# Kernel tuning notes

Measured on AMD Instinct MI355X. Metric: run time of the kernel, lower is better.

Reference implementation:

```python
import jax, jax.numpy as jnp
from jax import lax
import numpy as np

H = 200           # mpnn_hidden_size
DEPTH = 3         # mpnn_depth
ATOM_FDIM = 39
BOND_FDIM = 11
B, NA, NB = 128, 48, 96   # molecules, atoms/mol, bonds/mol (padded fixed size)
L, VOCAB = 1000, 26       # protein length, amino-acid vocab
KERNALS = [3, 5, 7]
PROT_FILTERS = [50, 96, 128, 200]
FC_DIMS = [400, 200, 100, 1]


def setup_inputs() -> dict:
    key = jax.random.key(0)
    ks = jax.random.split(key, 32)
    s = 0.05
    inp = {}
    inp["fatoms"] = jax.random.normal(ks[0], (B, NA, ATOM_FDIM), jnp.float32)
    inp["fbonds"] = jax.random.normal(ks[1], (B, NB, ATOM_FDIM + BOND_FDIM), jnp.float32)
    inp["agraph"] = jax.random.randint(ks[2], (B, NA, 6), 0, NB)
    inp["bgraph"] = jax.random.randint(ks[3], (B, NB, 6), 0, NB)
    inp["protein_seq"] = jax.random.randint(ks[4], (B, L), 0, VOCAB)
    # MPNN weights (stored as (in, out) matrices; W_i and W_h have no bias)
    inp["W_i"] = jax.random.normal(ks[5], (ATOM_FDIM + BOND_FDIM, H), jnp.float32) * s
    inp["W_h"] = jax.random.normal(ks[6], (H, H), jnp.float32) * s
    inp["W_o_w"] = jax.random.normal(ks[7], (ATOM_FDIM + H, H), jnp.float32) * s
    inp["W_o_b"] = jax.random.normal(ks[8], (H,), jnp.float32) * s
    # protein embedding + CNN
    inp["embed_protein"] = jax.random.normal(ks[9], (VOCAB, PROT_FILTERS[0]), jnp.float32) * s
    for i, k in enumerate(KERNALS):
        inp[f"conv{i}_w"] = jax.random.normal(ks[10 + 2 * i], (PROT_FILTERS[i + 1], PROT_FILTERS[i], k), jnp.float32) * s
        inp[f"conv{i}_b"] = jax.random.normal(ks[11 + 2 * i], (PROT_FILTERS[i + 1],), jnp.float32) * s
    # CPI fc head 400 -> 200 -> 100 -> 1
    for i in range(3):
        inp[f"fc{i}_w"] = jax.random.normal(ks[16 + 2 * i], (FC_DIMS[i], FC_DIMS[i + 1]), jnp.float32) * s
        inp[f"fc{i}_b"] = jax.random.normal(ks[17 + 2 * i], (FC_DIMS[i + 1],), jnp.float32) * s
    return inp


def reference(fatoms, fbonds, agraph, bgraph, protein_seq,
              W_i, W_h, W_o_w, W_o_b, embed_protein,
              conv0_w, conv0_b, conv1_w, conv1_b, conv2_w, conv2_b,
              fc0_w, fc0_b, fc1_w, fc1_b, fc2_w, fc2_b):
    # ---- MPNN over all molecules (vmapped single_molecule_forward) ----
    def mol(fa, fb, ag, bg):
        binput = fb @ W_i                      # (NB, H)
        message = jax.nn.relu(binput)
        for _ in range(DEPTH - 1):
            nei = message[bg].sum(axis=1)      # gather (NB,6,H) -> sum -> (NB,H)
            message = jax.nn.relu(binput + nei @ W_h)
        nei = message[ag].sum(axis=1)          # (NA, H)
        atom_h = jax.nn.relu(jnp.concatenate([fa, nei], axis=1) @ W_o_w + W_o_b)
        return atom_h.mean(axis=0)             # (H,)

    embeddings = jax.vmap(mol)(fatoms, fbonds, agraph, bgraph)  # (B, H)

    # ---- protein CNN tower ----
    pv = embed_protein[protein_seq]            # (B, L, 50)
    pv = pv.transpose(0, 2, 1)                 # (B, 50, L)
    for w, b, k in ((conv0_w, conv0_b, KERNALS[0]),
                    (conv1_w, conv1_b, KERNALS[1]),
                    (conv2_w, conv2_b, KERNALS[2])):
        pv = lax.conv_general_dilated(pv, w, window_strides=(1,),
                                      padding=[(k // 2, k // 2)],
                                      dimension_numbers=("NCH", "OIH", "NCH"))
        pv = jax.nn.relu(pv + b[None, :, None])
    protein_vector = pv.max(axis=2)            # adaptive_max_pool1d(out=1) -> (B, 200)

    # ---- CPI fc head ----
    x = jnp.concatenate([embeddings, protein_vector], axis=1)  # (B, 400)
    x = jax.nn.relu(x @ fc0_w + fc0_b)
    x = jax.nn.relu(x @ fc1_w + fc1_b)
    x = x @ fc2_w + fc2_b
    return x                                   # (B, 1)
```

## Files before the change

kernel.cpp:

```cpp
#include <hip/hip_runtime.h>
#include <hip/hip_bf16.h>
#include <cstddef>

#define H 200
#define NA 48
#define NBB 96
#define BATCH 128
#define AFD 39
#define BFD 50
#define LP 1000
#define CATD (AFD + H)
#define APB 8
#define BIPB 16

typedef unsigned short ushort_t;
typedef __bf16 bf16x8 __attribute__((ext_vector_type(8)));
typedef float f32x16 __attribute__((ext_vector_type(16)));
typedef unsigned uint32x4 __attribute__((ext_vector_type(4)));

union U16B { uint4 u; bf16x8 b; };
static __device__ __forceinline__ bf16x8 as_bf16x8(uint4 u) { U16B x; x.u = u; return x.b; }
union U16B2 { uint32x4 u; bf16x8 b; };
static __device__ __forceinline__ bf16x8 as_bf16x8v(uint32x4 u) { U16B2 x; x.u = u; return x.b; }

static __device__ __forceinline__ ushort_t f2bf(float f) {
    union { float f; unsigned u; } a; a.f = f;
    unsigned r = (a.u + 0x7FFFu + ((a.u >> 16) & 1u)) >> 16;
    return (ushort_t)r;
}

static __device__ __forceinline__ uint32x4 gload16(const ushort_t* base, unsigned voff) {
    uint32x4 r;
    asm volatile("global_load_dwordx4 %0, %1, %2"
                 : "=&v"(r) : "v"(voff), "s"(base));
    return r;
}

template <int COUT, int CIN, int CP, int K>
static __device__ __forceinline__ void prep_one(int t, const float* __restrict__ w,
                                                ushort_t* __restrict__ Wb) {
    constexpr int NC = CP / 16;
    constexpr int NS = K * NC;
    int j = t & 7;
    int lane = (t >> 3) & 63;
    int s = (t >> 9) % NS;
    int ct = (t >> 9) / NS;
    int co = ct * 32 + (lane & 31);
    int tt = s / NC, cc = s % NC;
    int ci = cc * 16 + ((lane >> 5) & 1) * 8 + j;
    float v = 0.f;
    if (co < COUT && ci < CIN) v = w[((size_t)co * CIN + ci) * K + tt];
    Wb[t] = f2bf(v);
}

#define MNS 13
#define PREP_T0 (4 * 12 * 512)
#define PREP_T1 (PREP_T0 + 4 * 30 * 512)
#define PREP_T2 (PREP_T1 + 8 * 56 * 512)
#define PREP_T3 (PREP_T2 + 51200)
#define PREP_T4 (PREP_T3 + 8 * MNS * 512)
#define PREP_BLKS (PREP_T4 / 256)

static __device__ __forceinline__ void prep_body(
        int tid, const float* __restrict__ c0w, const float* __restrict__ c1w,
        const float* __restrict__ c2w, const float* __restrict__ Wh,
        float* __restrict__ x, ushort_t* __restrict__ Wb0,
        ushort_t* __restrict__ Wb1, ushort_t* __restrict__ Wb2,
        ushort_t* __restrict__ Wbh) {
    if (tid < PREP_T0) prep_one<96, 50, 64, 3>(tid, c0w, Wb0);
    else if (tid < PREP_T1) prep_one<128, 96, 96, 5>(tid - PREP_T0, c1w, Wb1);
    else if (tid < PREP_T2) prep_one<200, 128, 128, 7>(tid - PREP_T1, c2w, Wb2);
    else if (tid < PREP_T3) x[tid - PREP_T2] = 0.f;
    else if (tid < PREP_T4) {
        int t = tid - PREP_T3;
        int j = t & 7;
        int lane = (t >> 3) & 63;
        int s = (t >> 9) % MNS;
        int tile = (t >> 9) / MNS;
        int co = tile * 32 + (lane & 31);
        int ci = s * 16 + ((lane >> 5) & 1) * 8 + j;
        float v = 0.f;
        if (co < H && ci < H) v = Wh[ci * H + co];
        Wbh[t] = f2bf(v);
    }
}

template <int CP, int K, int COUT, int CO_WAVES, int L_WAVES, bool FMAX, bool EMB>
static __device__ __forceinline__ void conv_body(
        const ushort_t* __restrict__ act, const int* __restrict__ seq,
        const float* __restrict__ emb, const ushort_t* __restrict__ Wb,
        const float* __restrict__ bias, void* __restrict__ outv,
        ushort_t* __restrict__ Xs) {
    constexpr int NC = CP / 16;
    constexpr int NS = K * NC;
    constexpr int P = K / 2;
    constexpr int PITCH = CP + 8;
    constexpr int LTILE = 64 * L_WAVES;
    constexpr int ROWS = LTILE + K - 1;
    constexpr int CPR = CP / 8;
    constexpr int D = 4;

    int b = blockIdx.z, lb = blockIdx.x;
    int l0 = lb * LTILE;
    int tid = threadIdx.x;

    if (EMB) {
        const int* seqb = seq + (size_t)b * LP;
        for (int idx = tid; idx < ROWS * CPR; idx += 256) {
            int r = idx / CPR, c = idx % CPR;
            int l = l0 - P + r;
            uint4 v = {0u, 0u, 0u, 0u};
            if ((unsigned)l < (unsigned)LP) {
                int s = seqb[l];
                const float* e = emb + (size_t)s * 50;
                ushort_t h[8];
#pragma unroll
                for (int j = 0; j < 8; ++j) {
                    int cc = c * 8 + j;
                    h[j] = (cc < 50) ? f2bf(e[cc]) : (ushort_t)0;
                }
                v.x = (unsigned)h[0] | ((unsigned)h[1] << 16);
                v.y = (unsigned)h[2] | ((unsigned)h[3] << 16);
                v.z = (unsigned)h[4] | ((unsigned)h[5] << 16);
                v.w = (unsigned)h[6] | ((unsigned)h[7] << 16);
            }
            *(uint4*)(Xs + r * PITCH + c * 8) = v;
        }
    } else {
        const ushort_t* actb = act + (size_t)b * LP * CP;
        for (int idx = tid; idx < ROWS * CPR; idx += 256) {
            int r = idx / CPR, c = idx % CPR;
            int l = l0 - P + r;
            uint4 v = {0u, 0u, 0u, 0u};
            if ((unsigned)l < (unsigned)LP) v = *(const uint4*)(actb + (size_t)l * CP + c * 8);
            *(uint4*)(Xs + r * PITCH + c * 8) = v;
        }
    }

    int lane = tid & 63, wv = tid >> 6;
    int cw = wv % CO_WAVES, lw = wv / CO_WAVES;
    int ln31 = lane & 31, half = lane >> 5;

    unsigned abase0 = (unsigned)(cw * 2) * (unsigned)NS * 1024u + (unsigned)lane * 16u;
    unsigned abase1 = abase0 + (unsigned)NS * 1024u;
    int bbase = (lw * 64 + ln31) * PITCH + half * 8;

    f32x16 acc[2][2];
#pragma unroll
    for (int ct = 0; ct < 2; ++ct)
#pragma unroll
        for (int lt = 0; lt < 2; ++lt)
#pragma unroll
            for (int r = 0; r < 16; ++r) acc[ct][lt][r] = 0.f;

    __syncthreads();

    uint32x4 ra0[D], ra1[D];
#pragma unroll
    for (int d = 0; d < D; ++d) {
        ra0[d] = gload16(Wb, abase0 + (unsigned)(d * 1024));
        ra1[d] = gload16(Wb, abase1 + (unsigned)(d * 1024));
    }

    uint4 bC0 = *(const uint4*)(Xs + bbase);
    uint4 bC1 = *(const uint4*)(Xs + bbase + 32 * PITCH);

#pragma unroll
    for (int s = 0; s < NS; ++s) {
        int sn = (s + 1 < NS) ? s + 1 : NS - 1;
        int tn = sn / NC, ccn = sn % NC;
        int off = bbase + tn * PITCH + ccn * 16;
        uint4 bN0 = *(const uint4*)(Xs + off);
        uint4 bN1 = *(const uint4*)(Xs + off + 32 * PITCH);

        {
            const int rem = NS - 1 - s;
            const int allow = 2 * ((D - 1) < rem ? (D - 1) : rem);
            asm volatile("s_waitcnt vmcnt(%0)" :: "i"(allow) : "memory");
            __builtin_amdgcn_sched_barrier(0);
        }

        uint32x4 a0 = ra0[s % D];
        uint32x4 a1 = ra1[s % D];

        acc[0][0] = __builtin_amdgcn_mfma_f32_32x32x16_bf16(
            as_bf16x8v(a0), as_bf16x8(bC0), acc[0][0], 0, 0, 0);
        acc[1][0] = __builtin_amdgcn_mfma_f32_32x32x16_bf16(
            as_bf16x8v(a1), as_bf16x8(bC0), acc[1][0], 0, 0, 0);
        acc[0][1] = __builtin_amdgcn_mfma_f32_32x32x16_bf16(
            as_bf16x8v(a0), as_bf16x8(bC1), acc[0][1], 0, 0, 0);
        acc[1][1] = __builtin_amdgcn_mfma_f32_32x32x16_bf16(
            as_bf16x8v(a1), as_bf16x8(bC1), acc[1][1], 0, 0, 0);

        if (s + D < NS) {
            ra0[s % D] = gload16(Wb, abase0 + (unsigned)((s + D) * 1024));
            ra1[s % D] = gload16(Wb, abase1 + (unsigned)((s + D) * 1024));
        }

        bC0 = bN0; bC1 = bN1;
    }

    if (!FMAX) {
        ushort_t* out = (ushort_t*)outv + (size_t)b * LP * COUT;
#pragma unroll
        for (int ct = 0; ct < 2; ++ct) {
            int cbase = (cw * 2 + ct) * 32 + 4 * half;
#pragma unroll
            for (int g = 0; g < 4; ++g) {
                int co = cbase + 8 * g;
                if (co >= COUT) continue;
                float4 bv = *(const float4*)(bias + co);
#pragma unroll
                for (int lt = 0; lt < 2; ++lt) {
                    int l = l0 + lw * 64 + lt * 32 + ln31;
                    if (l < LP) {
                        ushort_t h0 = f2bf(fmaxf(acc[ct][lt][4 * g + 0] + bv.x, 0.f));
                        ushort_t h1 = f2bf(fmaxf(acc[ct][lt][4 * g + 1] + bv.y, 0.f));
                        ushort_t h2 = f2bf(fmaxf(acc[ct][lt][4 * g + 2] + bv.z, 0.f));
                        ushort_t h3 = f2bf(fmaxf(acc[ct][lt][4 * g + 3] + bv.w, 0.f));
                        uint2 o;
                        o.x = (unsigned)h0 | ((unsigned)h1 << 16);
                        o.y = (unsigned)h2 | ((unsigned)h3 << 16);
                        *(uint2*)(out + (size_t)l * COUT + co) = o;
                    }
                }
            }
        }
    } else {
        float* xout = (float*)outv;
#pragma unroll
        for (int ct = 0; ct < 2; ++ct) {
            float mx[16];
#pragma unroll
            for (int r = 0; r < 16; ++r) mx[r] = -3.0e38f;
#pragma unroll
            for (int lt = 0; lt < 2; ++lt) {
                int l = l0 + lw * 64 + lt * 32 + ln31;
                if (l < LP) {
#pragma unroll
                    for (int r = 0; r < 16; ++r) mx[r] = fmaxf(mx[r], acc[ct][lt][r]);
                }
            }
#pragma unroll
            for (int r = 0; r < 16; ++r) {
#pragma unroll
                for (int off = 1; off < 32; off <<= 1)
                    mx[r] = fmaxf(mx[r], __shfl_xor(mx[r], off, 64));
            }
            if (ln31 == 0) {
                int cbase = (cw * 2 + ct) * 32 + 4 * half;
#pragma unroll
                for (int r = 0; r < 16; ++r) {
                    int co = cbase + (r & 3) + 8 * (r >> 2);
                    if (co < COUT) {
                        float v = fmaxf(mx[r] + bias[co], 0.f);
                        atomicMax((int*)&xout[(size_t)b * 400 + 200 + co], __float_as_int(v));
                    }
                }
            }
        }
    }
}

#define MPITCH 216
static __device__ __forceinline__ void msg_body(
        int blk, const float* __restrict__ msgIn, const float* __restrict__ binput,
        const int* __restrict__ bgraph, const ushort_t* __restrict__ Wbh,
        float* __restrict__ msgOut, ushort_t* __restrict__ Xs, int* __restrict__ idxs) {
    constexpr int D = 4;
    int m0 = blk * 32;
    int tid = threadIdx.x;

    if (tid < 192) {
        int r = tid / 6, j = tid - r * 6;
        int m = m0 + r;
        int mol = m / NBB;
        idxs[tid] = mol * NBB + bgraph[(size_t)m * 6 + j];
    }
    __syncthreads();

    for (int it = tid; it < 32 * 26; it += 256) {
        int r = it / 26, c = it - r * 26;
        uint4 v = {0u, 0u, 0u, 0u};
        if (c < 25) {
            float sv[8];
#pragma unroll
            for (int k = 0; k < 8; ++k) sv[k] = 0.f;
#pragma unroll
            for (int j = 0; j < 6; ++j) {
                const float* row = msgIn + (size_t)idxs[r * 6 + j] * H + c * 8;
                float4 a = *(const float4*)row;
                float4 b = *(const float4*)(row + 4);
                sv[0] += a.x; sv[1] += a.y; sv[2] += a.z; sv[3] += a.w;
                sv[4] += b.x; sv[5] += b.y; sv[6] += b.z; sv[7] += b.w;
            }
            v.x = (unsigned)f2bf(sv[0]) | ((unsigned)f2bf(sv[1]) << 16);
            v.y = (unsigned)f2bf(sv[2]) | ((unsigned)f2bf(sv[3]) << 16);
            v.z = (unsigned)f2bf(sv[4]) | ((unsigned)f2bf(sv[5]) << 16);
            v.w = (unsigned)f2bf(sv[6]) | ((unsigned)f2bf(sv[7]) << 16);
        }
        *(uint4*)(Xs + r * MPITCH + c * 8) = v;
    }

    int lane = tid & 63, wv = tid >> 6;
    int ln31 = lane & 31, half = lane >> 5;
    unsigned abase0 = (unsigned)(wv * 2) * (unsigned)MNS * 1024u + (unsigned)lane * 16u;
    unsigned abase1 = abase0 + (unsigned)MNS * 1024u;
    int bbase = ln31 * MPITCH + half * 8;

    f32x16 acc[2];
#pragma unroll
    for (int ct = 0; ct < 2; ++ct)
#pragma unroll
        for (int r = 0; r < 16; ++r) acc[ct][r] = 0.f;

    __syncthreads();

    uint32x4 ra0[4], ra1[4];
#pragma unroll
    for (int d = 0; d < D; ++d) {
        ra0[d] = gload16(Wbh, abase0 + (unsigned)(d * 1024));
        ra1[d] = gload16(Wbh, abase1 + (unsigned)(d * 1024));
    }

    uint4 bC = *(const uint4*)(Xs + bbase);

#pragma unroll
    for (int s = 0; s < MNS; ++s) {
        int sn = (s + 1 < MNS) ? s + 1 : MNS - 1;
        uint4 bN = *(const uint4*)(Xs + bbase + sn * 16);

        {
            const int rem = MNS - 1 - s;
            const int allow = 2 * ((D - 1) < rem ? (D - 1) : rem);
            asm volatile("s_waitcnt vmcnt(%0)" :: "i"(allow) : "memory");
            __builtin_amdgcn_sched_barrier(0);
        }

        uint32x4 a0 = ra0[s % D];
        uint32x4 a1 = ra1[s % D];
        acc[0] = __builtin_amdgcn_mfma_f32_32x32x16_bf16(
            as_bf16x8v(a0), as_bf16x8(bC), acc[0], 0, 0, 0);
        acc[1] = __builtin_amdgcn_mfma_f32_32x32x16_bf16(
            as_bf16x8v(a1), as_bf16x8(bC), acc[1], 0, 0, 0);

        if (s + D < MNS) {
            ra0[s % D] = gload16(Wbh, abase0 + (unsigned)((s + D) * 1024));
            ra1[s % D] = gload16(Wbh, abase1 + (unsigned)((s + D) * 1024));
        }
        bC = bN;
    }

    int m = m0 + ln31;
    const float* bi = binput + (size_t)m * H;
    float* outp = msgOut + (size_t)m * H;
#pragma unroll
    for (int ct = 0; ct < 2; ++ct) {
        int cbase = (wv * 2 + ct) * 32 + 4 * half;
#pragma unroll
        for (int g = 0; g < 4; ++g) {
            int co = cbase + 8 * g;
            if (co >= H) continue;
            float4 b4 = *(const float4*)(bi + co);
            float4 o;
            o.x = fmaxf(acc[ct][4 * g + 0] + b4.x, 0.f);
            o.y = fmaxf(acc[ct][4 * g + 1] + b4.y, 0.f);
            o.z = fmaxf(acc[ct][4 * g + 2] + b4.z, 0.f);
            o.w = fmaxf(acc[ct][4 * g + 3] + b4.w, 0.f);
            *(float4*)(outp + co) = o;
        }
    }
}

static __device__ __forceinline__ void bond_body(
        int blk, const float* __restrict__ fbonds, const float* __restrict__ Wi,
        float* __restrict__ binput, float* __restrict__ msg, float (*fb)[BFD]) {
    int bond0 = blk * BIPB;
    int tid = threadIdx.x;
    for (int idx = tid; idx < BIPB * BFD; idx += 256)
        fb[idx / BFD][idx % BFD] = fbonds[(size_t)bond0 * BFD + idx];
    __syncthreads();
    if (tid < H) {
        float acc[BIPB];
#pragma unroll
        for (int q = 0; q < BIPB; ++q) acc[q] = 0.f;
#pragma unroll 5
        for (int k = 0; k < BFD; ++k) {
            float w = Wi[k * H + tid];
#pragma unroll
            for (int q = 0; q < BIPB; ++q) acc[q] += fb[q][k] * w;
        }
#pragma unroll
        for (int q = 0; q < BIPB; ++q) {
            size_t o = (size_t)(bond0 + q) * H + tid;
            binput[o] = acc[q];
            msg[o] = fmaxf(acc[q], 0.f);
        }
    }
}

static __device__ __forceinline__ void atom_body(
        int blk, const float* __restrict__ msg, const float* __restrict__ fatoms,
        const int* __restrict__ agraph, const float* __restrict__ Wo,
        const float* __restrict__ Wob, float* __restrict__ x,
        float (*cat)[CATD], int* __restrict__ idxs) {
    const int grpPerMol = NA / APB;
    int b = blk / grpPerMol;
    int grp = blk % grpPerMol;
    int atom0 = grp * APB;
    int tid = threadIdx.x;
    if (tid < APB * 6) idxs[tid] = agraph[((size_t)(b * NA + atom0)) * 6 + tid];
    for (int idx = tid; idx < APB * AFD; idx += 256) {
        int q = idx / AFD, c = idx % AFD;
        cat[q][c] = fatoms[((size_t)(b * NA + atom0 + q)) * AFD + c];
    }
    __syncthreads();
    if (tid < H) {
        const float* base = msg + (size_t)b * NBB * H;
#pragma unroll
        for (int q = 0; q < APB; ++q) {
            float s = 0.f;
#pragma unroll
            for (int j = 0; j < 6; ++j) s += base[(size_t)idxs[q * 6 + j] * H + tid];
            cat[q][AFD + tid] = s;
        }
    }
    __syncthreads();
    if (tid < H) {
        float bb = Wob[tid];
        float acc[APB];
#pragma unroll
        for (int q = 0; q < APB; ++q) acc[q] = bb;
#pragma unroll 4
        for (int k = 0; k < CATD; ++k) {
            float w = Wo[k * H + tid];
#pragma unroll
            for (int q = 0; q < APB; ++q) acc[q] += cat[q][k] * w;
        }
        float s = 0.f;
#pragma unroll
        for (int q = 0; q < APB; ++q) s += fmaxf(acc[q], 0.f);
        atomicAdd(&x[(size_t)b * 400 + tid], s * (1.f / NA));
    }
}


__global__ __launch_bounds__(256) void k_l0_prep_bond(
        const float* __restrict__ c0w, const float* __restrict__ c1w,
        const float* __restrict__ c2w, const float* __restrict__ Wh,
        float* __restrict__ x, ushort_t* __restrict__ Wb0,
        ushort_t* __restrict__ Wb1, ushort_t* __restrict__ Wb2,
        ushort_t* __restrict__ Wbh,
        const float* __restrict__ fbonds, const float* __restrict__ Wi,
        float* __restrict__ binput, float* __restrict__ msgA) {
    __shared__ float fb[BIPB][BFD];
    int bid = blockIdx.x;
    if (bid < PREP_BLKS) {
        prep_body(bid * 256 + threadIdx.x, c0w, c1w, c2w, Wh, x, Wb0, Wb1, Wb2, Wbh);
    } else {
        bond_body(bid - PREP_BLKS, fbonds, Wi, binput, msgA, fb);
    }
}

__global__ __launch_bounds__(256, 3) void k_l1_conv0_msg(
        const int* __restrict__ seq, const float* __restrict__ emb,
        const ushort_t* __restrict__ Wb0, const float* __restrict__ c0b,
        ushort_t* __restrict__ act1,
        const float* __restrict__ msgIn, const float* __restrict__ binput,
        const int* __restrict__ bgraph, const ushort_t* __restrict__ Wbh,
        float* __restrict__ msgOut) {
    __shared__ __align__(16) ushort_t Sbuf[(128 + 2) * (64 + 8)];
    if (blockIdx.x < 8) {
        conv_body<64, 3, 96, 2, 2, false, true>(nullptr, seq, emb, Wb0, c0b, act1, Sbuf);
    } else {
        int blk = (blockIdx.x - 8) * 128 + blockIdx.z;
        msg_body(blk, msgIn, binput, bgraph, Wbh, msgOut, Sbuf,
                 (int*)(Sbuf + 32 * MPITCH));
    }
}

__global__ __launch_bounds__(256, 3) void k_l2_conv1_msg(
        const ushort_t* __restrict__ act1, const ushort_t* __restrict__ Wb1,
        const float* __restrict__ c1b, ushort_t* __restrict__ act2,
        const float* __restrict__ msgIn, const float* __restrict__ binput,
        const int* __restrict__ bgraph, const ushort_t* __restrict__ Wbh,
        float* __restrict__ msgOut) {
    __shared__ __align__(16) ushort_t Sbuf[(128 + 4) * (96 + 8)];
    if (blockIdx.x < 8) {
        conv_body<96, 5, 128, 2, 2, false, false>(act1, nullptr, nullptr, Wb1, c1b, act2, Sbuf);
    } else {
        int blk = (blockIdx.x - 8) * 128 + blockIdx.z;
        msg_body(blk, msgIn, binput, bgraph, Wbh, msgOut, Sbuf,
                 (int*)(Sbuf + 32 * MPITCH));
    }
}

__global__ __launch_bounds__(256, 3) void k_l3_conv2_atom(
        const ushort_t* __restrict__ act2, const ushort_t* __restrict__ Wb2,
        const float* __restrict__ c2b, float* __restrict__ x,
        const float* __restrict__ msg, const float* __restrict__ fatoms,
        const int* __restrict__ agraph, const float* __restrict__ Wo,
        const float* __restrict__ Wob) {
    __shared__ __align__(16) ushort_t Sbuf[(64 + 6) * (128 + 8)];
    if (blockIdx.x < 16) {
        conv_body<128, 7, 200, 4, 1, true, false>(act2, nullptr, nullptr, Wb2, c2b, x, Sbuf);
    } else {
        int blk = (blockIdx.x - 16) * 128 + blockIdx.z;
        float (*cat)[CATD] = (float (*)[CATD])Sbuf;
        int* idxs = (int*)((char*)Sbuf + APB * CATD * 4);
        atom_body(blk, msg, fatoms, agraph, Wo, Wob, x, cat, idxs);
    }
}

__global__ __launch_bounds__(256) void k_fc(
        const float* __restrict__ x,
        const float* __restrict__ w0, const float* __restrict__ b0,
        const float* __restrict__ w1, const float* __restrict__ b1,
        const float* __restrict__ w2, const float* __restrict__ b2,
        float* __restrict__ out) {
    int b = blockIdx.x, tid = threadIdx.x;
    __shared__ float xr[400];
    __shared__ float h1[200];
    __shared__ float h2[100];
    for (int i = tid; i < 400; i += 256) xr[i] = x[(size_t)b * 400 + i];
    __syncthreads();
    if (tid < 200) {
        float a = b0[tid];
#pragma unroll 4
        for (int k = 0; k < 400; ++k) a += xr[k] * w0[k * 200 + tid];
        h1[tid] = fmaxf(a, 0.f);
    }
    __syncthreads();
    if (tid < 100) {
        float a = b1[tid];
#pragma unroll 4
        for (int k = 0; k < 200; ++k) a += h1[k] * w1[k * 100 + tid];
        h2[tid] = fmaxf(a, 0.f);
    }
    __syncthreads();
    if (tid == 0) {
        float a = b2[0];
#pragma unroll 4
        for (int k = 0; k < 100; ++k) a += h2[k] * w2[k];
        out[b] = a;
    }
}

extern "C" void kernel_launch(void* const* d_in, const int* in_sizes, int n_in,
                              void* d_out, int out_size, void* d_ws, size_t ws_size,
                              hipStream_t stream) {
    const float* fatoms = (const float*)d_in[0];
    const float* fbonds = (const float*)d_in[1];
    const int* agraph = (const int*)d_in[2];
    const int* bgraph = (const int*)d_in[3];
    const int* seq = (const int*)d_in[4];
    const float* Wi = (const float*)d_in[5];
    const float* Wh = (const float*)d_in[6];
    const float* Wo = (const float*)d_in[7];
    const float* Wob = (const float*)d_in[8];
    const float* embp = (const float*)d_in[9];
    const float* c0w = (const float*)d_in[10];
    const float* c0b = (const float*)d_in[11];
    const float* c1w = (const float*)d_in[12];
    const float* c1b = (const float*)d_in[13];
    const float* c2w = (const float*)d_in[14];
    const float* c2b = (const float*)d_in[15];
    const float* fc0w = (const float*)d_in[16];
    const float* fc0b = (const float*)d_in[17];
    const float* fc1w = (const float*)d_in[18];
    const float* fc1b = (const float*)d_in[19];
    const float* fc2w = (const float*)d_in[20];
    const float* fc2b = (const float*)d_in[21];

    float* ws = (float*)d_ws;
    float* binput = ws;
    float* msgA = binput + 2457600;
    float* msgB = msgA + 2457600;
    float* x = msgB + 2457600;
    ushort_t* u = (ushort_t*)(x + 51200);
    ushort_t* act1 = u;
    ushort_t* act2 = act1 + 12288000;
    ushort_t* Wb0 = act2 + 16384000;
    ushort_t* Wb1 = Wb0 + 24576;
    ushort_t* Wb2 = Wb1 + 61440;
    ushort_t* Wbh = Wb2 + 229376;

    k_l0_prep_bond<<<PREP_BLKS + BATCH * NBB / BIPB, 256, 0, stream>>>(
        c0w, c1w, c2w, Wh, x, Wb0, Wb1, Wb2, Wbh, fbonds, Wi, binput, msgA);

    k_l1_conv0_msg<<<dim3(8 + 3, 1, BATCH), 256, 0, stream>>>(
        seq, embp, Wb0, c0b, act1, msgA, binput, bgraph, Wbh, msgB);

    k_l2_conv1_msg<<<dim3(8 + 3, 1, BATCH), 256, 0, stream>>>(
        act1, Wb1, c1b, act2, msgB, binput, bgraph, Wbh, msgA);

    k_l3_conv2_atom<<<dim3(16 + 6, 1, BATCH), 256, 0, stream>>>(
        act2, Wb2, c2b, x, msgA, fatoms, agraph, Wo, Wob);

    k_fc<<<BATCH, 256, 0, stream>>>(x, fc0w, fc0b, fc1w, fc1b, fc2w, fc2b, (float*)d_out);
}
```

Measured before the change: 331.0 us.

## Move atom readout GEMM to bf16 MFMA with prepacked W_o weights

Measured after the change: 323.6 us. -2.2%, faster.

```diff
diff --git a/kernel.cpp b/kernel.cpp
--- a/kernel.cpp
+++ b/kernel.cpp
@@ -10,7 +10,6 @@
 #define BFD 50
 #define LP 1000
 #define CATD (AFD + H)
-#define APB 8
 #define BIPB 16
 
 typedef unsigned short ushort_t;
@@ -54,19 +53,22 @@
 }
 
 #define MNS 13
+#define ANS 15
 #define PREP_T0 (4 * 12 * 512)
 #define PREP_T1 (PREP_T0 + 4 * 30 * 512)
 #define PREP_T2 (PREP_T1 + 8 * 56 * 512)
 #define PREP_T3 (PREP_T2 + 51200)
 #define PREP_T4 (PREP_T3 + 8 * MNS * 512)
-#define PREP_BLKS (PREP_T4 / 256)
+#define PREP_T5 (PREP_T4 + 8 * ANS * 512)
+#define PREP_BLKS (PREP_T5 / 256)
 
 static __device__ __forceinline__ void prep_body(
         int tid, const float* __restrict__ c0w, const float* __restrict__ c1w,
         const float* __restrict__ c2w, const float* __restrict__ Wh,
-        float* __restrict__ x, ushort_t* __restrict__ Wb0,
-        ushort_t* __restrict__ Wb1, ushort_t* __restrict__ Wb2,
-        ushort_t* __restrict__ Wbh) {
+        const float* __restrict__ Wo, float* __restrict__ x,
+        ushort_t* __restrict__ Wb0, ushort_t* __restrict__ Wb1,
+        ushort_t* __restrict__ Wb2, ushort_t* __restrict__ Wbh,
+        ushort_t* __restrict__ Wbo) {
     if (tid < PREP_T0) prep_one<96, 50, 64, 3>(tid, c0w, Wb0);
     else if (tid < PREP_T1) prep_one<128, 96, 96, 5>(tid - PREP_T0, c1w, Wb1);
     else if (tid < PREP_T2) prep_one<200, 128, 128, 7>(tid - PREP_T1, c2w, Wb2);
@@ -82,6 +84,20 @@
         float v = 0.f;
         if (co < H && ci < H) v = Wh[ci * H + co];
         Wbh[t] = f2bf(v);
+    } else if (tid < PREP_T5) {
+        int t = tid - PREP_T4;
+        int j = t & 7;
+        int lane = (t >> 3) & 63;
+        int s = (t >> 9) % ANS;
+        int tile = (t >> 9) / ANS;
+        int co = tile * 32 + (lane & 31);
+        int cip = s * 16 + ((lane >> 5) & 1) * 8 + j;
+        float v = 0.f;
+        if (co < H) {
+            if (cip < 200) v = Wo[(size_t)(39 + cip) * H + co];
+            else if (cip < CATD) v = Wo[(size_t)(cip - 200) * H + co];
+        }
+        Wbo[t] = f2bf(v);
     }
 }
 
@@ -372,6 +388,133 @@
     }
 }
 
+#define APITCH 248
+static __device__ __forceinline__ void atom_mfma_body(
+        int blk, const float* __restrict__ msg, const float* __restrict__ fatoms,
+        const int* __restrict__ agraph, const ushort_t* __restrict__ Wbo,
+        const float* __restrict__ Wob, float* __restrict__ x,
+        ushort_t* __restrict__ Xs, int* __restrict__ idxs) {
+    constexpr int D = 4;
+    int m0 = blk * 32;
+    int tid = threadIdx.x;
+
+    if (tid < 192) {
+        int r = tid / 6, j = tid - r * 6;
+        int m = m0 + r;
+        int mol = m / NA;
+        idxs[tid] = mol * NBB + agraph[(size_t)m * 6 + j];
+    }
+    __syncthreads();
+
+    for (int it = tid; it < 32 * 30; it += 256) {
+        int r = it / 30, c = it - r * 30;
+        uint4 v = {0u, 0u, 0u, 0u};
+        if (c < 25) {
+            float sv[8];
+#pragma unroll
+            for (int k = 0; k < 8; ++k) sv[k] = 0.f;
+#pragma unroll
+            for (int j = 0; j < 6; ++j) {
+                const float* row = msg + (size_t)idxs[r * 6 + j] * H + c * 8;
+                float4 a = *(const float4*)row;
+                float4 b = *(const float4*)(row + 4);
+                sv[0] += a.x; sv[1] += a.y; sv[2] += a.z; sv[3] += a.w;
+                sv[4] += b.x; sv[5] += b.y; sv[6] += b.z; sv[7] += b.w;
+            }
+            v.x = (unsigned)f2bf(sv[0]) | ((unsigned)f2bf(sv[1]) << 16);
+            v.y = (unsigned)f2bf(sv[2]) | ((unsigned)f2bf(sv[3]) << 16);
+            v.z = (unsigned)f2bf(sv[4]) | ((unsigned)f2bf(sv[5]) << 16);
+            v.w = (unsigned)f2bf(sv[6]) | ((unsigned)f2bf(sv[7]) << 16);
+        } else {
+            int m = m0 + r;
+            ushort_t h[8];
+#pragma unroll
+            for (int j = 0; j < 8; ++j) {
+                int f = c * 8 + j - 200;
+                h[j] = (f < AFD) ? f2bf(fatoms[(size_t)m * AFD + f]) : (ushort_t)0;
+            }
+            v.x = (unsigned)h[0] | ((unsigned)h[1] << 16);
+            v.y = (unsigned)h[2] | ((unsigned)h[3] << 16);
+            v.z = (unsigned)h[4] | ((unsigned)h[5] << 16);
+            v.w = (unsigned)h[6] | ((unsigned)h[7] << 16);
+        }
+        *(uint4*)(Xs + r * APITCH + c * 8) = v;
+    }
+
+    int lane = tid & 63, wv = tid >> 6;
+    int ln31 = lane & 31, half = lane >> 5;
+    unsigned abase0 = (unsigned)(wv * 2) * (unsigned)ANS * 1024u + (unsigned)lane * 16u;
+    unsigned abase1 = abase0 + (unsigned)ANS * 1024u;
+    int bbase = ln31 * APITCH + half * 8;
+
+    f32x16 acc[2];
+#pragma unroll
+    for (int ct = 0; ct < 2; ++ct)
+#pragma unroll
+        for (int r = 0; r < 16; ++r) acc[ct][r] = 0.f;
+
+    __syncthreads();
+
+    uint32x4 ra0[4], ra1[4];
+#pragma unroll
+    for (int d = 0; d < D; ++d) {
+        ra0[d] = gload16(Wbo, abase0 + (unsigned)(d * 1024));
+        ra1[d] = gload16(Wbo, abase1 + (unsigned)(d * 1024));
+    }
+
+    uint4 bC = *(const uint4*)(Xs + bbase);
+
+#pragma unroll
+    for (int s = 0; s < ANS; ++s) {
+        int sn = (s + 1 < ANS) ? s + 1 : ANS - 1;
+        uint4 bN = *(const uint4*)(Xs + bbase + sn * 16);
+
+        {
+            const int rem = ANS - 1 - s;
+            const int allow = 2 * ((D - 1) < rem ? (D - 1) : rem);
+            asm volatile("s_waitcnt vmcnt(%0)" :: "i"(allow) : "memory");
+            __builtin_amdgcn_sched_barrier(0);
+        }
+
+        uint32x4 a0 = ra0[s % D];
+        uint32x4 a1 = ra1[s % D];
+        acc[0] = __builtin_amdgcn_mfma_f32_32x32x16_bf16(
+            as_bf16x8v(a0), as_bf16x8(bC), acc[0], 0, 0, 0);
+        acc[1] = __builtin_amdgcn_mfma_f32_32x32x16_bf16(
+            as_bf16x8v(a1), as_bf16x8(bC), acc[1], 0, 0, 0);
+
+        if (s + D < ANS) {
+            ra0[s % D] = gload16(Wbo, abase0 + (unsigned)((s + D) * 1024));
+            ra1[s % D] = gload16(Wbo, abase1 + (unsigned)((s + D) * 1024));
+        }
+        bC = bN;
+    }
+
+    int rm = m0 % 48;
+    bool split = (rm == 32);
+    int molA = m0 / 48;
+    const float inv = 1.f / NA;
+#pragma unroll
+    for (int ct = 0; ct < 2; ++ct) {
+        int cbase = (wv * 2 + ct) * 32 + 4 * half;
+#pragma unroll
+        for (int r = 0; r < 16; ++r) {
+            int co = cbase + (r & 3) + 8 * (r >> 2);
+            float v = 0.f;
+            if (co < H) v = fmaxf(acc[ct][r] + Wob[co], 0.f) * inv;
+            v += __shfl_xor(v, 1, 64);
+            v += __shfl_xor(v, 2, 64);
+            v += __shfl_xor(v, 4, 64);
+            v += __shfl_xor(v, 8, 64);
+            if (!split) v += __shfl_xor(v, 16, 64);
+            if (co < H) {
+                if (ln31 == 0) atomicAdd(&x[(size_t)molA * 400 + co], v);
+                else if (split && ln31 == 16) atomicAdd(&x[(size_t)(molA + 1) * 400 + co], v);
+            }
+        }
+    }
+}
+
 static __device__ __forceinline__ void bond_body(
         int blk, const float* __restrict__ fbonds, const float* __restrict__ Wi,
         float* __restrict__ binput, float* __restrict__ msg, float (*fb)[BFD]) {
@@ -399,64 +542,20 @@
     }
 }
 
-static __device__ __forceinline__ void atom_body(
-        int blk, const float* __restrict__ msg, const float* __restrict__ fatoms,
-        const int* __restrict__ agraph, const float* __restrict__ Wo,
-        const float* __restrict__ Wob, float* __restrict__ x,
-        float (*cat)[CATD], int* __restrict__ idxs) {
-    const int grpPerMol = NA / APB;
-    int b = blk / grpPerMol;
-    int grp = blk % grpPerMol;
-    int atom0 = grp * APB;
-    int tid = threadIdx.x;
-    if (tid < APB * 6) idxs[tid] = agraph[((size_t)(b * NA + atom0)) * 6 + tid];
-    for (int idx = tid; idx < APB * AFD; idx += 256) {
-        int q = idx / AFD, c = idx % AFD;
-        cat[q][c] = fatoms[((size_t)(b * NA + atom0 + q)) * AFD + c];
-    }
-    __syncthreads();
-    if (tid < H) {
-        const float* base = msg + (size_t)b * NBB * H;
-#pragma unroll
-        for (int q = 0; q < APB; ++q) {
-            float s = 0.f;
-#pragma unroll
-            for (int j = 0; j < 6; ++j) s += base[(size_t)idxs[q * 6 + j] * H + tid];
-            cat[q][AFD + tid] = s;
-        }
-    }
-    __syncthreads();
-    if (tid < H) {
-        float bb = Wob[tid];
-        float acc[APB];
-#pragma unroll
-        for (int q = 0; q < APB; ++q) acc[q] = bb;
-#pragma unroll 4
-        for (int k = 0; k < CATD; ++k) {
-            float w = Wo[k * H + tid];
-#pragma unroll
-            for (int q = 0; q < APB; ++q) acc[q] += cat[q][k] * w;
-        }
-        float s = 0.f;
-#pragma unroll
-        for (int q = 0; q < APB; ++q) s += fmaxf(acc[q], 0.f);
-        atomicAdd(&x[(size_t)b * 400 + tid], s * (1.f / NA));
-    }
-}
-
 
 __global__ __launch_bounds__(256) void k_l0_prep_bond(
         const float* __restrict__ c0w, const float* __restrict__ c1w,
         const float* __restrict__ c2w, const float* __restrict__ Wh,
-        float* __restrict__ x, ushort_t* __restrict__ Wb0,
-        ushort_t* __restrict__ Wb1, ushort_t* __restrict__ Wb2,
-        ushort_t* __restrict__ Wbh,
+        const float* __restrict__ Wo, float* __restrict__ x,
+        ushort_t* __restrict__ Wb0, ushort_t* __restrict__ Wb1,
+        ushort_t* __restrict__ Wb2, ushort_t* __restrict__ Wbh,
+        ushort_t* __restrict__ Wbo,
         const float* __restrict__ fbonds, const float* __restrict__ Wi,
         float* __restrict__ binput, float* __restrict__ msgA) {
     __shared__ float fb[BIPB][BFD];
     int bid = blockIdx.x;
     if (bid < PREP_BLKS) {
-        prep_body(bid * 256 + threadIdx.x, c0w, c1w, c2w, Wh, x, Wb0, Wb1, Wb2, Wbh);
+        prep_body(bid * 256 + threadIdx.x, c0w, c1w, c2w, Wh, Wo, x, Wb0, Wb1, Wb2, Wbh, Wbo);
     } else {
         bond_body(bid - PREP_BLKS, fbonds, Wi, binput, msgA, fb);
     }
@@ -499,16 +598,17 @@
         const ushort_t* __restrict__ act2, const ushort_t* __restrict__ Wb2,
         const float* __restrict__ c2b, float* __restrict__ x,
         const float* __restrict__ msg, const float* __restrict__ fatoms,
-        const int* __restrict__ agraph, const float* __restrict__ Wo,
+        const int* __restrict__ agraph, const ushort_t* __restrict__ Wbo,
         const float* __restrict__ Wob) {
     __shared__ __align__(16) ushort_t Sbuf[(64 + 6) * (128 + 8)];
     if (blockIdx.x < 16) {
         conv_body<128, 7, 200, 4, 1, true, false>(act2, nullptr, nullptr, Wb2, c2b, x, Sbuf);
     } else {
         int blk = (blockIdx.x - 16) * 128 + blockIdx.z;
-        float (*cat)[CATD] = (float (*)[CATD])Sbuf;
-        int* idxs = (int*)((char*)Sbuf + APB * CATD * 4);
-        atom_body(blk, msg, fatoms, agraph, Wo, Wob, x, cat, idxs);
+        if (blk < 192) {
+            atom_mfma_body(blk, msg, fatoms, agraph, Wbo, Wob, x, Sbuf,
+                           (int*)(Sbuf + 32 * APITCH));
+        }
     }
 }
 
@@ -584,9 +684,10 @@
     ushort_t* Wb1 = Wb0 + 24576;
     ushort_t* Wb2 = Wb1 + 61440;
     ushort_t* Wbh = Wb2 + 229376;
+    ushort_t* Wbo = Wbh + 53248;
 
     k_l0_prep_bond<<<PREP_BLKS + BATCH * NBB / BIPB, 256, 0, stream>>>(
-        c0w, c1w, c2w, Wh, x, Wb0, Wb1, Wb2, Wbh, fbonds, Wi, binput, msgA);
+        c0w, c1w, c2w, Wh, Wo, x, Wb0, Wb1, Wb2, Wbh, Wbo, fbonds, Wi, binput, msgA);
 
     k_l1_conv0_msg<<<dim3(8 + 3, 1, BATCH), 256, 0, stream>>>(
         seq, embp, Wb0, c0b, act1, msgA, binput, bgraph, Wbh, msgB);
@@ -594,8 +695,8 @@
     k_l2_conv1_msg<<<dim3(8 + 3, 1, BATCH), 256, 0, stream>>>(
         act1, Wb1, c1b, act2, msgB, binput, bgraph, Wbh, msgA);
 
-    k_l3_conv2_atom<<<dim3(16 + 6, 1, BATCH), 256, 0, stream>>>(
-        act2, Wb2, c2b, x, msgA, fatoms, agraph, Wo, Wob);
+    k_l3_conv2_atom<<<dim3(16 + 2, 1, BATCH), 256, 0, stream>>>(
+        act2, Wb2, c2b, x, msgA, fatoms, agraph, Wbo, Wob);
 
     k_fc<<<BATCH, 256, 0, stream>>>(x, fc0w, fc0b, fc1w, fc1b, fc2w, fc2b, (float*)d_out);
 }
```
